# Kernel optimization log

Measured on AMD Instinct MI355X. Metric: run time of the kernel, lower is better.

The kernel has to match this reference:

```python
import jax, jax.numpy as jnp
import numpy as np

V, D, K = 50000, 300, 50      # vocab, embed_dim, dim_latent (topics)
B, S, N, L = 32, 8192, 128, 64  # batch, doc len, segments/doc, max seg len (=stride)


def setup_inputs() -> dict:
    key = jax.random.key(0)
    k0, k1, k2, k3, k4, k5 = jax.random.split(key, 6)
    embedding = jax.random.normal(k0, (V, D), jnp.float32) * 0.02
    M_w = jax.random.normal(k1, (D, D), jnp.float32) / np.sqrt(D).astype(np.float32)
    W_w = jax.random.normal(k2, (K, D), jnp.float32) / np.sqrt(D).astype(np.float32)
    T_w = jax.random.normal(k3, (D, K), jnp.float32) / np.sqrt(K).astype(np.float32)
    input_tensor = jax.random.randint(k4, (B, S), 0, V)
    # non-overlapping segments with stride L; ragged lengths in [8, L]
    seg_starts = jnp.broadcast_to(jnp.arange(N, dtype=jnp.int32) * L, (B, N))
    seg_lens = jax.random.randint(k5, (B, N), 8, L + 1)
    return {"embedding": embedding, "M_w": M_w, "W_w": W_w, "T_w": T_w,
            "input_tensor": input_tensor, "seg_starts": seg_starts, "seg_lens": seg_lens}


def reference(embedding, M_w, W_w, T_w, input_tensor, seg_starts, seg_lens):
    # Build padded segment token grid + mask (vectorized version of the
    # per-batch Python loop in the original forward).
    offs = jnp.arange(L)
    pos = seg_starts[..., None] + offs                       # [B,N,L]
    mask = (offs < seg_lens[..., None]).astype(embedding.dtype)  # [B,N,L]
    tok = jnp.take_along_axis(input_tensor, pos.reshape(B, N * L), axis=1).reshape(B, N, L)
    sub_emb = embedding[tok] * mask[..., None]               # [B,N,L,D] (zeros at pad)
    # masked mean over segment tokens
    y = sub_emb.sum(axis=2) / jnp.maximum(mask.sum(axis=2), 1.0)[..., None]  # [B,N,D]
    # attention score: (M @ e_l) . y, masked softmax
    esc = jnp.einsum('bnld,ed,bne->bnl', sub_emb, M_w, y)    # M(x) = x @ M_w.T
    esc = jnp.where(mask > 0, esc, -1e9)
    alpha = jax.nn.softmax(esc, axis=-1)                     # [B,N,L]
    z = jnp.einsum('bnl,bnld->bnd', alpha, sub_emb)          # [B,N,D]
    p = jax.nn.softmax(z @ W_w.T, axis=-1)                   # [B,N,K]
    r = p @ T_w.T                                            # [B,N,D]
    return y, z, p, r
```

## Files before the change

kernel.cpp:

```cpp
#include <hip/hip_runtime.h>

#define DD 300
#define KK 50
#define BB 32
#define SS 8192
#define NN 128
#define LL 64
#define NSEG (BB * NN)
#define TM 8
#define NTU 320
#define TTP 304
#define TTR 64

__device__ __forceinline__ float wave_sum(float v) {
    #pragma unroll
    for (int m = 32; m; m >>= 1) v += __shfl_xor(v, m, 64);
    return v;
}
__device__ __forceinline__ float wave_max(float v) {
    #pragma unroll
    for (int m = 32; m; m >>= 1) v = fmaxf(v, __shfl_xor(v, m, 64));
    return v;
}
__device__ __forceinline__ float dot4(float4 a, float4 b) {
    return a.x * b.x + a.y * b.y + a.z * b.z + a.w * b.w;
}
__device__ __forceinline__ void fma4(float4& acc, float s, float4 v) {
    acc.x += s * v.x; acc.y += s * v.y; acc.z += s * v.z; acc.w += s * v.w;
}

__device__ __forceinline__ void ld_rows(const float* __restrict__ emb, int tok, int len,
                                        int l0, int lane, bool bl, float4* A, float4* B) {
    #pragma unroll
    for (int i = 0; i < 4; ++i) {
        int lc = l0 + i; lc = (lc < len) ? lc : (len - 1);
        const int t = __shfl(tok, lc);
        const float4* r4 = (const float4*)(emb + (size_t)t * DD);
        A[i] = r4[lane];
        if (bl) B[i] = r4[11 + lane];
    }
}
__device__ __forceinline__ void ld_wrows(const float* __restrict__ W, int rmax, int pitch,
                                         int k0, int lane, bool bl, float4* A, float4* B) {
    #pragma unroll
    for (int i = 0; i < 4; ++i) {
        int kc = k0 + i; kc = (kc < rmax) ? kc : rmax;
        const float4* r4 = (const float4*)(W + (size_t)kc * pitch);
        A[i] = r4[lane];
        if (bl) B[i] = r4[11 + lane];
    }
}

__global__ __launch_bounds__(TTP) void k_tt(const float* __restrict__ T_w,
                                            float* __restrict__ Tt) {
    const int k = blockIdx.x;
    const int d = threadIdx.x;
    float v = 0.f;
    if (k < KK && d < DD) v = T_w[(size_t)d * KK + k];
    Tt[(size_t)k * TTP + d] = v;
}

__global__ __launch_bounds__(256) void k_y1(
    const float* __restrict__ emb,
    const int*   __restrict__ tokens,
    const int*   __restrict__ seg_starts,
    const int*   __restrict__ seg_lens,
    float* __restrict__ out_y)
{
    const int wave = threadIdx.x >> 6;
    const int lane = threadIdx.x & 63;
    const int seg  = blockIdx.x * 4 + wave;
    const int len  = seg_lens[seg];
    const int base = (seg >> 7) * SS + seg_starts[seg];
    const int tok  = tokens[base + lane];
    const bool bl  = (lane >= 53);

    float4 A0[4], B0[4], A1[4], B1[4];
    #pragma unroll
    for (int i = 0; i < 4; ++i) {
        B0[i] = make_float4(0.f, 0.f, 0.f, 0.f);
        B1[i] = make_float4(0.f, 0.f, 0.f, 0.f);
    }
    float4 aA = make_float4(0.f, 0.f, 0.f, 0.f);
    float4 aB = make_float4(0.f, 0.f, 0.f, 0.f);

    const int len8 = (len + 7) & ~7;
    ld_rows(emb, tok, len, 0, lane, bl, A0, B0);
    for (int l0 = 0; l0 < len8; l0 += 8) {
        ld_rows(emb, tok, len, l0 + 4, lane, bl, A1, B1);
        #pragma unroll
        for (int i = 0; i < 4; ++i) {
            const float m = (l0 + i < len) ? 1.f : 0.f;
            fma4(aA, m, A0[i]); fma4(aB, m, B0[i]);
        }
        ld_rows(emb, tok, len, l0 + 8, lane, bl, A0, B0);
        #pragma unroll
        for (int i = 0; i < 4; ++i) {
            const float m = (l0 + 4 + i < len) ? 1.f : 0.f;
            fma4(aA, m, A1[i]); fma4(aB, m, B1[i]);
        }
    }
    const float inv = 1.f / (float)len;
    aA.x *= inv; aA.y *= inv; aA.z *= inv; aA.w *= inv;
    aB.x *= inv; aB.y *= inv; aB.z *= inv; aB.w *= inv;
    float4* yo = (float4*)(out_y + (size_t)seg * DD);
    yo[lane] = aA;
    if (bl) yo[11 + lane] = aB;
}

__global__ __launch_bounds__(NTU) void k_u(
    const float* __restrict__ y,
    const float* __restrict__ M_w,
    float* __restrict__ u)
{
    const int tid  = threadIdx.x;
    const int row0 = blockIdx.x * TM;
    if (tid >= DD) return;

    float acc[TM];
    #pragma unroll
    for (int r = 0; r < TM; ++r) acc[r] = 0.f;

    #pragma unroll 5
    for (int e = 0; e < DD; ++e) {
        const float m = M_w[(size_t)e * DD + tid];
        #pragma unroll
        for (int r = 0; r < TM; ++r)
            acc[r] += m * y[(size_t)(row0 + r) * DD + e];
    }
    #pragma unroll
    for (int r = 0; r < TM; ++r)
        u[(size_t)(row0 + r) * DD + tid] = acc[r];
}

__global__ __launch_bounds__(256) void k_rest(
    const float* __restrict__ emb,
    const float* __restrict__ W_w,
    const float* __restrict__ T_w,
    const float* __restrict__ Tt,
    const int    use_tt,
    const int*   __restrict__ tokens,
    const int*   __restrict__ seg_starts,
    const int*   __restrict__ seg_lens,
    const float* __restrict__ u_ws,
    float* __restrict__ out_z,
    float* __restrict__ out_p,
    float* __restrict__ out_r)
{
    const int wave = threadIdx.x >> 6;
    const int lane = threadIdx.x & 63;
    const int seg  = blockIdx.x * 4 + wave;
    const int len  = seg_lens[seg];
    const int base = (seg >> 7) * SS + seg_starts[seg];
    const int tok  = tokens[base + lane];
    const bool bl  = (lane >= 53);

    const float4* u4 = (const float4*)(u_ws + (size_t)seg * DD);
    const float4 U0 = u4[lane];
    float4 U1 = make_float4(0.f, 0.f, 0.f, 0.f);
    if (bl) U1 = u4[11 + lane];

    float4 A0[4], B0[4], A1[4], B1[4];
    #pragma unroll
    for (int i = 0; i < 4; ++i) {
        B0[i] = make_float4(0.f, 0.f, 0.f, 0.f);
        B1[i] = make_float4(0.f, 0.f, 0.f, 0.f);
    }

    float esc = 0.f;
    const int len8 = (len + 7) & ~7;
    ld_rows(emb, tok, len, 0, lane, bl, A0, B0);
    for (int l0 = 0; l0 < len8; l0 += 8) {
        ld_rows(emb, tok, len, l0 + 4, lane, bl, A1, B1);
        {
            float d0 = dot4(A0[0], U0) + dot4(B0[0], U1);
            float d1 = dot4(A0[1], U0) + dot4(B0[1], U1);
            float d2 = dot4(A0[2], U0) + dot4(B0[2], U1);
            float d3 = dot4(A0[3], U0) + dot4(B0[3], U1);
            d0 = wave_sum(d0); d1 = wave_sum(d1); d2 = wave_sum(d2); d3 = wave_sum(d3);
            esc = (lane == l0 + 0) ? d0 : esc;
            esc = (lane == l0 + 1) ? d1 : esc;
            esc = (lane == l0 + 2) ? d2 : esc;
            esc = (lane == l0 + 3) ? d3 : esc;
        }
        ld_rows(emb, tok, len, l0 + 8, lane, bl, A0, B0);
        {
            float d0 = dot4(A1[0], U0) + dot4(B1[0], U1);
            float d1 = dot4(A1[1], U0) + dot4(B1[1], U1);
            float d2 = dot4(A1[2], U0) + dot4(B1[2], U1);
            float d3 = dot4(A1[3], U0) + dot4(B1[3], U1);
            d0 = wave_sum(d0); d1 = wave_sum(d1); d2 = wave_sum(d2); d3 = wave_sum(d3);
            esc = (lane == l0 + 4) ? d0 : esc;
            esc = (lane == l0 + 5) ? d1 : esc;
            esc = (lane == l0 + 6) ? d2 : esc;
            esc = (lane == l0 + 7) ? d3 : esc;
        }
    }

    const float v  = (lane < len) ? esc : -INFINITY;
    const float mx = wave_max(v);
    const float ex = (lane < len) ? __expf(v - mx) : 0.f;
    const float sm = wave_sum(ex);
    const float alpha = ex / sm;

    float4 zA = make_float4(0.f, 0.f, 0.f, 0.f);
    float4 zB = make_float4(0.f, 0.f, 0.f, 0.f);
    ld_rows(emb, tok, len, 0, lane, bl, A0, B0);
    for (int l0 = 0; l0 < len8; l0 += 8) {
        ld_rows(emb, tok, len, l0 + 4, lane, bl, A1, B1);
        #pragma unroll
        for (int i = 0; i < 4; ++i) {
            const float a = __shfl(alpha, l0 + i);
            fma4(zA, a, A0[i]); fma4(zB, a, B0[i]);
        }
        ld_rows(emb, tok, len, l0 + 8, lane, bl, A0, B0);
        #pragma unroll
        for (int i = 0; i < 4; ++i) {
            const float a = __shfl(alpha, l0 + 4 + i);
            fma4(zA, a, A1[i]); fma4(zB, a, B1[i]);
        }
    }
    {
        float4* zo = (float4*)(out_z + (size_t)seg * DD);
        zo[lane] = zA;
        if (bl) zo[11 + lane] = zB;
    }

    float sc = 0.f;
    ld_wrows(W_w, KK - 1, DD, 0, lane, bl, A0, B0);
    for (int k0 = 0; k0 < 56; k0 += 8) {
        ld_wrows(W_w, KK - 1, DD, k0 + 4, lane, bl, A1, B1);
        {
            float t0 = dot4(A0[0], zA) + dot4(B0[0], zB);
            float t1 = dot4(A0[1], zA) + dot4(B0[1], zB);
            float t2 = dot4(A0[2], zA) + dot4(B0[2], zB);
            float t3 = dot4(A0[3], zA) + dot4(B0[3], zB);
            t0 = wave_sum(t0); t1 = wave_sum(t1); t2 = wave_sum(t2); t3 = wave_sum(t3);
            sc = (lane == k0 + 0) ? t0 : sc;
            sc = (lane == k0 + 1) ? t1 : sc;
            sc = (lane == k0 + 2) ? t2 : sc;
            sc = (lane == k0 + 3) ? t3 : sc;
        }
        ld_wrows(W_w, KK - 1, DD, k0 + 8, lane, bl, A0, B0);
        {
            float t0 = dot4(A1[0], zA) + dot4(B1[0], zB);
            float t1 = dot4(A1[1], zA) + dot4(B1[1], zB);
            float t2 = dot4(A1[2], zA) + dot4(B1[2], zB);
            float t3 = dot4(A1[3], zA) + dot4(B1[3], zB);
            t0 = wave_sum(t0); t1 = wave_sum(t1); t2 = wave_sum(t2); t3 = wave_sum(t3);
            sc = (lane == k0 + 4) ? t0 : sc;
            sc = (lane == k0 + 5) ? t1 : sc;
            sc = (lane == k0 + 6) ? t2 : sc;
            sc = (lane == k0 + 7) ? t3 : sc;
        }
    }
    const float vk  = (lane < KK) ? sc : -INFINITY;
    const float mxk = wave_max(vk);
    const float ek  = (lane < KK) ? __expf(vk - mxk) : 0.f;
    const float smk = wave_sum(ek);
    const float p   = ek / smk;
    if (lane < KK) out_p[(size_t)seg * KK + lane] = p;

    float4 rA = make_float4(0.f, 0.f, 0.f, 0.f);
    float4 rB = make_float4(0.f, 0.f, 0.f, 0.f);
    if (use_tt) {
        ld_wrows(Tt, TTR - 1, TTP, 0, lane, bl, A0, B0);
        for (int k0 = 0; k0 < 56; k0 += 8) {
            ld_wrows(Tt, TTR - 1, TTP, k0 + 4, lane, bl, A1, B1);
            #pragma unroll
            for (int i = 0; i < 4; ++i) {
                const float pk = __shfl(p, k0 + i);
                fma4(rA, pk, A0[i]); fma4(rB, pk, B0[i]);
            }
            ld_wrows(Tt, TTR - 1, TTP, k0 + 8, lane, bl, A0, B0);
            #pragma unroll
            for (int i = 0; i < 4; ++i) {
                const float pk = __shfl(p, k0 + 4 + i);
                fma4(rA, pk, A1[i]); fma4(rB, pk, B1[i]);
            }
        }
    } else {
        const int dA = 4 * lane, dB = 44 + 4 * lane;
        for (int k = 0; k < KK; ++k) {
            const float pk = __shfl(p, k);
            rA.x += pk * T_w[(size_t)(dA + 0) * KK + k];
            rA.y += pk * T_w[(size_t)(dA + 1) * KK + k];
            rA.z += pk * T_w[(size_t)(dA + 2) * KK + k];
            rA.w += pk * T_w[(size_t)(dA + 3) * KK + k];
            if (bl) {
                rB.x += pk * T_w[(size_t)(dB + 0) * KK + k];
                rB.y += pk * T_w[(size_t)(dB + 1) * KK + k];
                rB.z += pk * T_w[(size_t)(dB + 2) * KK + k];
                rB.w += pk * T_w[(size_t)(dB + 3) * KK + k];
            }
        }
    }
    {
        float4* ro = (float4*)(out_r + (size_t)seg * DD);
        ro[lane] = rA;
        if (bl) ro[11 + lane] = rB;
    }
}

extern "C" void kernel_launch(void* const* d_in, const int* in_sizes, int n_in,
                              void* d_out, int out_size, void* d_ws, size_t ws_size,
                              hipStream_t stream) {
    const float* emb        = (const float*)d_in[0];
    const float* M_w        = (const float*)d_in[1];
    const float* W_w        = (const float*)d_in[2];
    const float* T_w        = (const float*)d_in[3];
    const int*   tokens     = (const int*)d_in[4];
    const int*   seg_starts = (const int*)d_in[5];
    const int*   seg_lens   = (const int*)d_in[6];

    float* out   = (float*)d_out;
    float* out_y = out;
    float* out_z = out + (size_t)NSEG * DD;
    float* out_p = out + (size_t)2 * NSEG * DD;
    float* out_r = out + (size_t)2 * NSEG * DD + (size_t)NSEG * KK;

    float* u_ws = (float*)d_ws;
    float* Tt   = u_ws + (size_t)NSEG * DD;
    const size_t need = ((size_t)NSEG * DD + (size_t)TTR * TTP) * sizeof(float);
    const int use_tt = (ws_size >= need) ? 1 : 0;

    if (use_tt)
        hipLaunchKernelGGL(k_tt, dim3(TTR), dim3(TTP), 0, stream, T_w, Tt);
    hipLaunchKernelGGL(k_y1, dim3(NSEG / 4), dim3(256), 0, stream,
                       emb, tokens, seg_starts, seg_lens, out_y);
    hipLaunchKernelGGL(k_u, dim3(NSEG / TM), dim3(NTU), 0, stream,
                       out_y, M_w, u_ws);
    hipLaunchKernelGGL(k_rest, dim3(NSEG / 4), dim3(256), 0, stream,
                       emb, W_w, T_w, Tt, use_tt, tokens, seg_starts, seg_lens,
                       u_ws, out_z, out_p, out_r);
}
```

Before: 212.7 us.

## Fuse attention scoring and weighted sum with online softmax in one pass

```diff
diff --git a/kernel.cpp b/kernel.cpp
--- a/kernel.cpp
+++ b/kernel.cpp
@@ -7,7 +7,7 @@
 #define NN 128
 #define LL 64
 #define NSEG (BB * NN)
-#define TM 8
+#define TMU 8
 #define NTU 320
 #define TTP 304
 #define TTR 64
@@ -27,6 +27,9 @@
 }
 __device__ __forceinline__ void fma4(float4& acc, float s, float4 v) {
     acc.x += s * v.x; acc.y += s * v.y; acc.z += s * v.z; acc.w += s * v.w;
+}
+__device__ __forceinline__ void scale4(float4& a, float s) {
+    a.x *= s; a.y *= s; a.z *= s; a.w *= s;
 }
 
 __device__ __forceinline__ void ld_rows(const float* __restrict__ emb, int tok, int len,
@@ -60,16 +63,15 @@
     Tt[(size_t)k * TTP + d] = v;
 }
 
-__global__ __launch_bounds__(256) void k_y1(
+__global__ __launch_bounds__(256, 4) void k_y1(
     const float* __restrict__ emb,
     const int*   __restrict__ tokens,
     const int*   __restrict__ seg_starts,
     const int*   __restrict__ seg_lens,
     float* __restrict__ out_y)
 {
-    const int wave = threadIdx.x >> 6;
     const int lane = threadIdx.x & 63;
-    const int seg  = blockIdx.x * 4 + wave;
+    const int seg  = blockIdx.x * 4 + (threadIdx.x >> 6);
     const int len  = seg_lens[seg];
     const int base = (seg >> 7) * SS + seg_starts[seg];
     const int tok  = tokens[base + lane];
@@ -101,8 +103,7 @@
         }
     }
     const float inv = 1.f / (float)len;
-    aA.x *= inv; aA.y *= inv; aA.z *= inv; aA.w *= inv;
-    aB.x *= inv; aB.y *= inv; aB.z *= inv; aB.w *= inv;
+    scale4(aA, inv); scale4(aB, inv);
     float4* yo = (float4*)(out_y + (size_t)seg * DD);
     yo[lane] = aA;
     if (bl) yo[11 + lane] = aB;
@@ -114,26 +115,26 @@
     float* __restrict__ u)
 {
     const int tid  = threadIdx.x;
-    const int row0 = blockIdx.x * TM;
+    const int row0 = blockIdx.x * TMU;
     if (tid >= DD) return;
 
-    float acc[TM];
-    #pragma unroll
-    for (int r = 0; r < TM; ++r) acc[r] = 0.f;
+    float acc[TMU];
+    #pragma unroll
+    for (int r = 0; r < TMU; ++r) acc[r] = 0.f;
 
     #pragma unroll 5
     for (int e = 0; e < DD; ++e) {
         const float m = M_w[(size_t)e * DD + tid];
         #pragma unroll
-        for (int r = 0; r < TM; ++r)
+        for (int r = 0; r < TMU; ++r)
             acc[r] += m * y[(size_t)(row0 + r) * DD + e];
     }
     #pragma unroll
-    for (int r = 0; r < TM; ++r)
+    for (int r = 0; r < TMU; ++r)
         u[(size_t)(row0 + r) * DD + tid] = acc[r];
 }
 
-__global__ __launch_bounds__(256) void k_rest(
+__global__ __launch_bounds__(256, 4) void k_rest(
     const float* __restrict__ emb,
     const float* __restrict__ W_w,
     const float* __restrict__ T_w,
@@ -147,9 +148,8 @@
     float* __restrict__ out_p,
     float* __restrict__ out_r)
 {
-    const int wave = threadIdx.x >> 6;
     const int lane = threadIdx.x & 63;
-    const int seg  = blockIdx.x * 4 + wave;
+    const int seg  = blockIdx.x * 4 + (threadIdx.x >> 6);
     const int len  = seg_lens[seg];
     const int base = (seg >> 7) * SS + seg_starts[seg];
     const int tok  = tokens[base + lane];
@@ -167,59 +167,48 @@
         B1[i] = make_float4(0.f, 0.f, 0.f, 0.f);
     }
 
-    float esc = 0.f;
+    float m = -INFINITY, s = 0.f;
+    float4 zA = make_float4(0.f, 0.f, 0.f, 0.f);
+    float4 zB = make_float4(0.f, 0.f, 0.f, 0.f);
+
+#define PROC4(A, B, BASE)                                                        \
+    {                                                                            \
+        float d0 = wave_sum(dot4(A[0], U0) + dot4(B[0], U1));                    \
+        float d1 = wave_sum(dot4(A[1], U0) + dot4(B[1], U1));                    \
+        float d2 = wave_sum(dot4(A[2], U0) + dot4(B[2], U1));                    \
+        float d3 = wave_sum(dot4(A[3], U0) + dot4(B[3], U1));                    \
+        const float e0 = ((BASE) + 0 < len) ? d0 : -INFINITY;                    \
+        const float e1 = ((BASE) + 1 < len) ? d1 : -INFINITY;                    \
+        const float e2 = ((BASE) + 2 < len) ? d2 : -INFINITY;                    \
+        const float e3 = ((BASE) + 3 < len) ? d3 : -INFINITY;                    \
+        const float g = fmaxf(fmaxf(e0, e1), fmaxf(e2, e3));                     \
+        if (g > m) {                                                             \
+            const float sc = __expf(m - g);      \
+            s *= sc; scale4(zA, sc); scale4(zB, sc); m = g;                      \
+        }                                                                        \
+        const float w0 = ((BASE) + 0 < len) ? __expf(d0 - m) : 0.f;              \
+        const float w1 = ((BASE) + 1 < len) ? __expf(d1 - m) : 0.f;              \
+        const float w2 = ((BASE) + 2 < len) ? __expf(d2 - m) : 0.f;              \
+        const float w3 = ((BASE) + 3 < len) ? __expf(d3 - m) : 0.f;              \
+        s += w0 + w1 + w2 + w3;                                                  \
+        fma4(zA, w0, A[0]); fma4(zB, w0, B[0]);                                  \
+        fma4(zA, w1, A[1]); fma4(zB, w1, B[1]);                                  \
+        fma4(zA, w2, A[2]); fma4(zB, w2, B[2]);                                  \
+        fma4(zA, w3, A[3]); fma4(zB, w3, B[3]);                                  \
+    }
+
     const int len8 = (len + 7) & ~7;
     ld_rows(emb, tok, len, 0, lane, bl, A0, B0);
     for (int l0 = 0; l0 < len8; l0 += 8) {
         ld_rows(emb, tok, len, l0 + 4, lane, bl, A1, B1);
-        {
-            float d0 = dot4(A0[0], U0) + dot4(B0[0], U1);
-            float d1 = dot4(A0[1], U0) + dot4(B0[1], U1);
-            float d2 = dot4(A0[2], U0) + dot4(B0[2], U1);
-            float d3 = dot4(A0[3], U0) + dot4(B0[3], U1);
-            d0 = wave_sum(d0); d1 = wave_sum(d1); d2 = wave_sum(d2); d3 = wave_sum(d3);
-            esc = (lane == l0 + 0) ? d0 : esc;
-            esc = (lane == l0 + 1) ? d1 : esc;
-            esc = (lane == l0 + 2) ? d2 : esc;
-            esc = (lane == l0 + 3) ? d3 : esc;
-        }
+        PROC4(A0, B0, l0)
         ld_rows(emb, tok, len, l0 + 8, lane, bl, A0, B0);
-        {
-            float d0 = dot4(A1[0], U0) + dot4(B1[0], U1);
-            float d1 = dot4(A1[1], U0) + dot4(B1[1], U1);
-            float d2 = dot4(A1[2], U0) + dot4(B1[2], U1);
-            float d3 = dot4(A1[3], U0) + dot4(B1[3], U1);
-            d0 = wave_sum(d0); d1 = wave_sum(d1); d2 = wave_sum(d2); d3 = wave_sum(d3);
-            esc = (lane == l0 + 4) ? d0 : esc;
-            esc = (lane == l0 + 5) ? d1 : esc;
-            esc = (lane == l0 + 6) ? d2 : esc;
-            esc = (lane == l0 + 7) ? d3 : esc;
-        }
-    }
-
-    const float v  = (lane < len) ? esc : -INFINITY;
-    const float mx = wave_max(v);
-    const float ex = (lane < len) ? __expf(v - mx) : 0.f;
-    const float sm = wave_sum(ex);
-    const float alpha = ex / sm;
-
-    float4 zA = make_float4(0.f, 0.f, 0.f, 0.f);
-    float4 zB = make_float4(0.f, 0.f, 0.f, 0.f);
-    ld_rows(emb, tok, len, 0, lane, bl, A0, B0);
-    for (int l0 = 0; l0 < len8; l0 += 8) {
-        ld_rows(emb, tok, len, l0 + 4, lane, bl, A1, B1);
-        #pragma unroll
-        for (int i = 0; i < 4; ++i) {
-            const float a = __shfl(alpha, l0 + i);
-            fma4(zA, a, A0[i]); fma4(zB, a, B0[i]);
-        }
-        ld_rows(emb, tok, len, l0 + 8, lane, bl, A0, B0);
-        #pragma unroll
-        for (int i = 0; i < 4; ++i) {
-            const float a = __shfl(alpha, l0 + 4 + i);
-            fma4(zA, a, A1[i]); fma4(zB, a, B1[i]);
-        }
-    }
+        PROC4(A1, B1, l0 + 4)
+    }
+#undef PROC4
+
+    const float invs = 1.f / s;
+    scale4(zA, invs); scale4(zB, invs);
     {
         float4* zo = (float4*)(out_z + (size_t)seg * DD);
         zo[lane] = zA;
@@ -231,11 +220,10 @@
     for (int k0 = 0; k0 < 56; k0 += 8) {
         ld_wrows(W_w, KK - 1, DD, k0 + 4, lane, bl, A1, B1);
         {
-            float t0 = dot4(A0[0], zA) + dot4(B0[0], zB);
-            float t1 = dot4(A0[1], zA) + dot4(B0[1], zB);
-            float t2 = dot4(A0[2], zA) + dot4(B0[2], zB);
-            float t3 = dot4(A0[3], zA) + dot4(B0[3], zB);
-            t0 = wave_sum(t0); t1 = wave_sum(t1); t2 = wave_sum(t2); t3 = wave_sum(t3);
+            float t0 = wave_sum(dot4(A0[0], zA) + dot4(B0[0], zB));
+            float t1 = wave_sum(dot4(A0[1], zA) + dot4(B0[1], zB));
+            float t2 = wave_sum(dot4(A0[2], zA) + dot4(B0[2], zB));
+            float t3 = wave_sum(dot4(A0[3], zA) + dot4(B0[3], zB));
             sc = (lane == k0 + 0) ? t0 : sc;
             sc = (lane == k0 + 1) ? t1 : sc;
             sc = (lane == k0 + 2) ? t2 : sc;
@@ -243,11 +231,10 @@
         }
         ld_wrows(W_w, KK - 1, DD, k0 + 8, lane, bl, A0, B0);
         {
-            float t0 = dot4(A1[0], zA) + dot4(B1[0], zB);
-            float t1 = dot4(A1[1], zA) + dot4(B1[1], zB);
-            float t2 = dot4(A1[2], zA) + dot4(B1[2], zB);
-            float t3 = dot4(A1[3], zA) + dot4(B1[3], zB);
-            t0 = wave_sum(t0); t1 = wave_sum(t1); t2 = wave_sum(t2); t3 = wave_sum(t3);
+            float t0 = wave_sum(dot4(A1[0], zA) + dot4(B1[0], zB));
+            float t1 = wave_sum(dot4(A1[1], zA) + dot4(B1[1], zB));
+            float t2 = wave_sum(dot4(A1[2], zA) + dot4(B1[2], zB));
+            float t3 = wave_sum(dot4(A1[3], zA) + dot4(B1[3], zB));
             sc = (lane == k0 + 4) ? t0 : sc;
             sc = (lane == k0 + 5) ? t1 : sc;
             sc = (lane == k0 + 6) ? t2 : sc;
@@ -328,7 +315,7 @@
         hipLaunchKernelGGL(k_tt, dim3(TTR), dim3(TTP), 0, stream, T_w, Tt);
     hipLaunchKernelGGL(k_y1, dim3(NSEG / 4), dim3(256), 0, stream,
                        emb, tokens, seg_starts, seg_lens, out_y);
-    hipLaunchKernelGGL(k_u, dim3(NSEG / TM), dim3(NTU), 0, stream,
+    hipLaunchKernelGGL(k_u, dim3(NSEG / TMU), dim3(NTU), 0, stream,
                        out_y, M_w, u_ws);
     hipLaunchKernelGGL(k_rest, dim3(NSEG / 4), dim3(256), 0, stream,
                        emb, W_w, T_w, Tt, use_tt, tokens, seg_starts, seg_lens,
```

Result: slower. 365.0 us (+71.6%).
